# Performance work log

Measured on AMD Instinct MI355X. Metric: run time of the kernel, lower is better.

Reference implementation:

```python
import jax, jax.numpy as jnp
import numpy as np

NUM_GROUPS = 9
POWER_P = 4.0
B = 8192

def setup_inputs() -> dict:
    key = jax.random.key(0)
    k1, k2, k3 = jax.random.split(key, 3)
    return {
        "logits_tox": jax.random.normal(k1, (B, 1), dtype=jnp.float32),
        "y_tox": jax.random.uniform(k2, (B, 1), dtype=jnp.float32),
        "y_id": jax.random.uniform(k3, (B, NUM_GROUPS), dtype=jnp.float32),
    }

def reference(logits_tox, y_tox, y_id):
    logits = logits_tox[:, 0]                      # [B]
    is_toxic = y_tox[:, 0] >= 0.5                  # [B] bool
    # D[i, j] = softplus(-(logits[i] - logits[j])) = softplus(logits[j] - logits[i])
    # row index i plays the 'pos' role, column index j plays the 'neg' role.
    D = jax.nn.softplus(logits[None, :] - logits[:, None])  # [B, B]

    in_group = (y_id >= 0.5).T                     # [G, B]
    tox = is_toxic[None, :]                        # [1, B]
    dt = logits.dtype
    sub_pos = (in_group & tox).astype(dt)          # [G, B]
    sub_neg = (in_group & ~tox).astype(dt)
    bg_pos = (~in_group & tox).astype(dt)
    bg_neg = (~in_group & ~tox).astype(dt)

    # three pair types: (sub_pos, sub_neg), (bg_pos, sub_neg), (sub_pos, bg_neg)
    pos_masks = jnp.stack([sub_pos, bg_pos, sub_pos])   # [3, G, B]
    neg_masks = jnp.stack([sub_neg, sub_neg, bg_neg])   # [3, G, B]

    num = jnp.einsum('tgi,ij,tgj->tg', pos_masks, D, neg_masks)  # [3, G]
    cnt = pos_masks.sum(-1) * neg_masks.sum(-1)                  # [3, G] n_pos*n_neg
    valid = cnt > 0                                              # pair type contributes only if both sides nonempty
    type_loss = num / jnp.maximum(cnt, 1.0)

    n_valid = valid.astype(dt).sum(0)                            # [G]
    group_loss = (type_loss * valid.astype(dt)).sum(0) / jnp.maximum(n_valid, 1.0)
    gv = (n_valid > 0).astype(dt)                                # [G] group validity
    n_groups = jnp.maximum(gv.sum(), 1.0)

    # power-mean aggregation (power_p = 4 > 1)
    mean_p = (jnp.power(group_loss, POWER_P) * gv).sum() / n_groups
    loss = jnp.power(mean_p, 1.0 / POWER_P)
    return jnp.where(gv.sum() > 0, loss, jnp.array(0.0, dt))
```

## Files before the change

kernel.cpp:

```cpp
#include <hip/hip_runtime.h>
#include <math.h>

#define NG 9
#define NBLK 1024
#define JT 16
#define LOG2E 1.4426950408889634f
#define LN2   0.6931471805599453f

__global__ __launch_bounds__(256) void k_classify(
    const float* __restrict__ logits, const float* __restrict__ ytox,
    const float* __restrict__ yid, int B, int* __restrict__ cnts,
    float2* __restrict__ iLM, float2* __restrict__ jLM) {

    __shared__ int wT[4], wN[4], offT[4], offN[4], bT, bN;
    __shared__ int gT[4][NG], gN[4][NG];

    const int tid = threadIdx.x, lane = tid & 63, wave = tid >> 6;
    const int row = blockIdx.x * 256 + tid;
    const bool v = row < B;

    float l = 0.f; bool tox = false, non = false; int m = 0;
    if (v) {
        l = logits[row] * LOG2E;
        tox = ytox[row] >= 0.5f;
        non = !tox;
#pragma unroll
        for (int g = 0; g < NG; ++g)
            if (yid[row * NG + g] >= 0.5f) m |= 1 << g;
    }

    const unsigned long long bTox = __ballot(tox), bNon = __ballot(non);
    const unsigned long long lt = (1ull << lane) - 1ull;
    const int pT = __popcll(bTox & lt), pN = __popcll(bNon & lt);
    if (lane == 0) { wT[wave] = __popcll(bTox); wN[wave] = __popcll(bNon); }
#pragma unroll
    for (int g = 0; g < NG; ++g) {
        const unsigned long long bt = __ballot(tox && ((m >> g) & 1));
        const unsigned long long bn = __ballot(non && ((m >> g) & 1));
        if (lane == 0) { gT[wave][g] = __popcll(bt); gN[wave][g] = __popcll(bn); }
    }
    __syncthreads();
    if (tid == 0) {
        int a = 0, b = 0;
#pragma unroll
        for (int w = 0; w < 4; ++w) { offT[w] = a; a += wT[w]; offN[w] = b; b += wN[w]; }
        bT = atomicAdd(&cnts[0], a);
        bN = atomicAdd(&cnts[1], b);
    }
    __syncthreads();
    if (tox) iLM[bT + offT[wave] + pT] = make_float2(l, __int_as_float(m));
    if (non) jLM[bN + offN[wave] + pN] = make_float2(l, __int_as_float(m));
    if (tid < NG)
        atomicAdd(&cnts[2 + tid], gT[0][tid] + gT[1][tid] + gT[2][tid] + gT[3][tid]);
    else if (tid < 2 * NG) {
        const int g = tid - NG;
        atomicAdd(&cnts[11 + g], gN[0][g] + gN[1][g] + gN[2][g] + gN[3][g]);
    }
}

__global__ __launch_bounds__(256, 4) void k_pairs(
    const int* __restrict__ cnts, const float2* __restrict__ iLM,
    const float2* __restrict__ jLM, float* __restrict__ part) {

    __shared__ float2 jS[JT];
    __shared__ float red[4][27];
    __shared__ float acc[27];

    const int tid = threadIdx.x, lane = tid & 63, wave = tid >> 6;
    const int blk = blockIdx.x;
    const int nI = cnts[0], nJ = cnts[1];
    const int nbI = (nI + 511) >> 9;
    const int nbJ = (nJ + JT - 1) / JT;
    const int nT = nbI * nbJ;

    if (tid < 27) acc[tid] = 0.f;

    float li0 = 1e30f, li1 = 1e30f;
    int mi0 = 0, mi1 = 0;
    float Ra0 = 0.f, Ra1 = 0.f;
    float Rg0[NG], Rg1[NG];
#pragma unroll
    for (int g = 0; g < NG; ++g) { Rg0[g] = 0.f; Rg1[g] = 0.f; }

    auto flush = [&]() {
#pragma unroll
        for (int g = 0; g < NG; ++g) {
            const bool i0 = (mi0 >> g) & 1, i1 = (mi1 >> g) & 1;
            float x0 = (i0 ? Rg0[g] : 0.f) + (i1 ? Rg1[g] : 0.f);
            float x1 = (i0 ? 0.f : Rg0[g]) + (i1 ? 0.f : Rg1[g]);
            float x2 = (i0 ? (Ra0 - Rg0[g]) : 0.f) + (i1 ? (Ra1 - Rg1[g]) : 0.f);
#pragma unroll
            for (int off = 32; off > 0; off >>= 1) {
                x0 += __shfl_xor(x0, off, 64);
                x1 += __shfl_xor(x1, off, 64);
                x2 += __shfl_xor(x2, off, 64);
            }
            if (lane == 0) {
                red[wave][g] = x0; red[wave][NG + g] = x1; red[wave][2 * NG + g] = x2;
            }
        }
        __syncthreads();
        if (tid < 27)
            acc[tid] += red[0][tid] + red[1][tid] + red[2][tid] + red[3][tid];
    };

    int prev_bi = -1;
    for (int t = blk; t < nT; t += NBLK) {
        const int bi = t % nbI, bj = t / nbI;
        if (bi != prev_bi) {
            if (prev_bi >= 0) flush();
            const int k0 = (bi << 9) + tid, k1 = k0 + 256;
            const float2 a0 = (k0 < nI) ? iLM[k0] : make_float2(1e30f, 0.f);
            const float2 a1 = (k1 < nI) ? iLM[k1] : make_float2(1e30f, 0.f);
            li0 = a0.x; mi0 = __float_as_int(a0.y);
            li1 = a1.x; mi1 = __float_as_int(a1.y);
            Ra0 = 0.f; Ra1 = 0.f;
#pragma unroll
            for (int g = 0; g < NG; ++g) { Rg0[g] = 0.f; Rg1[g] = 0.f; }
            prev_bi = bi;
        }
        const int jbeg = bj * JT;
        const int jcnt = min(JT, nJ - jbeg);
        __syncthreads();
        if (tid < jcnt) jS[tid] = jLM[jbeg + tid];
        __syncthreads();
#pragma unroll 4
        for (int k = 0; k < jcnt; ++k) {
            const float2 jv = jS[k];
            const float lj = jv.x;
            const int mj = __builtin_amdgcn_readfirstlane(__float_as_int(jv.y));
            const float s0 = __builtin_amdgcn_logf(1.f + __builtin_amdgcn_exp2f(lj - li0));
            const float s1 = __builtin_amdgcn_logf(1.f + __builtin_amdgcn_exp2f(lj - li1));
            Ra0 += s0; Ra1 += s1;
#pragma unroll
            for (int g = 0; g < NG; ++g) {
                const float bg = ((mj >> g) & 1) ? 1.f : 0.f;
                Rg0[g] = fmaf(bg, s0, Rg0[g]);
                Rg1[g] = fmaf(bg, s1, Rg1[g]);
            }
        }
    }
    if (prev_bi >= 0) flush();
    if (tid < 27) part[tid * NBLK + blk] = acc[tid];
}

__global__ __launch_bounds__(512) void k_final(
    const float* __restrict__ part, const int* __restrict__ cnts,
    float* __restrict__ out) {
    __shared__ float fin[27];
    const int tid = threadIdx.x, lane = tid & 63, wave = tid >> 6;
    for (int r = wave; r < 27; r += 8) {
        float s = 0.f;
#pragma unroll
        for (int q = 0; q < NBLK / 64; ++q) s += part[r * NBLK + (q << 6) + lane];
#pragma unroll
        for (int off = 32; off > 0; off >>= 1) s += __shfl_xor(s, off, 64);
        if (lane == 0) fin[r] = s * LN2;
    }
    __syncthreads();
    if (tid == 0) {
        const long long nT = cnts[0], nN = cnts[1];
        double accd = 0.0; int ngv = 0;
        for (int g = 0; g < NG; ++g) {
            const long long cT = cnts[2 + g], cN = cnts[11 + g];
            const long long c0 = cT * cN;
            const long long c1 = (nT - cT) * cN;
            const long long c2 = cT * (nN - cN);
            const double t0 = (double)fin[g]          / (double)(c0 > 0 ? c0 : 1);
            const double t1 = (double)fin[NG + g]     / (double)(c1 > 0 ? c1 : 1);
            const double t2 = (double)fin[2 * NG + g] / (double)(c2 > 0 ? c2 : 1);
            const int nv = (c0 > 0) + (c1 > 0) + (c2 > 0);
            const double gl = ((c0 > 0 ? t0 : 0.0) + (c1 > 0 ? t1 : 0.0) +
                               (c2 > 0 ? t2 : 0.0)) / (double)(nv > 0 ? nv : 1);
            if (nv > 0) { const double g2 = gl * gl; accd += g2 * g2; ++ngv; }
        }
        const double mp = accd / (double)(ngv > 0 ? ngv : 1);
        const double loss = sqrt(sqrt(mp));
        out[0] = (float)(ngv > 0 ? loss : 0.0);
    }
}

extern "C" void kernel_launch(void* const* d_in, const int* in_sizes, int n_in,
                              void* d_out, int out_size, void* d_ws, size_t ws_size,
                              hipStream_t stream) {
    const float* logits = (const float*)d_in[0];
    const float* ytox   = (const float*)d_in[1];
    const float* yid    = (const float*)d_in[2];
    const int B = in_sizes[0];

    char* ws = (char*)d_ws;
    int*    cnts = (int*)ws;
    float2* iLM  = (float2*)(ws + 128);
    float2* jLM  = (float2*)(ws + 128 + (size_t)B * 8);
    float*  part = (float*)(ws + 128 + (size_t)B * 16);

    hipMemsetAsync(cnts, 0, 20 * sizeof(int), stream);
    k_classify<<<dim3((B + 255) / 256), dim3(256), 0, stream>>>(
        logits, ytox, yid, B, cnts, iLM, jLM);
    k_pairs<<<dim3(NBLK), dim3(256), 0, stream>>>(cnts, iLM, jLM, part);
    k_final<<<dim3(1), dim3(512), 0, stream>>>(part, cnts, (float*)d_out);
}
```

Baseline: 92.08 us.

## Fuse classify, pair and final kernels into one cooperative kernel with grid syncs

Replaces the memset and three separate launches with a single cooperative kernel. Per-chunk counts and a shared-memory prefix scan replace the global atomics, and a binary search per element maps each i/j index into chunk-local compacted storage. The j tile grows from 16 to 32. The goal is to remove launch gaps and atomic contention, at the cost of two grid-wide barriers, a serial prefix scan in every block, and binary-search overhead on each load.

```diff
diff --git a/kernel.cpp b/kernel.cpp
--- a/kernel.cpp
+++ b/kernel.cpp
@@ -1,77 +1,97 @@
 #include <hip/hip_runtime.h>
+#include <hip/hip_cooperative_groups.h>
 #include <math.h>
+
+namespace cg = cooperative_groups;
 
 #define NG 9
 #define NBLK 1024
-#define JT 16
+#define CHROWS 256
+#define NCHMAX 1024
+#define JT 32
+#define ITILE 512
 #define LOG2E 1.4426950408889634f
 #define LN2   0.6931471805599453f
 
-__global__ __launch_bounds__(256) void k_classify(
+__global__ __launch_bounds__(256, 4) void k_fused(
     const float* __restrict__ logits, const float* __restrict__ ytox,
-    const float* __restrict__ yid, int B, int* __restrict__ cnts,
-    float2* __restrict__ iLM, float2* __restrict__ jLM) {
-
-    __shared__ int wT[4], wN[4], offT[4], offN[4], bT, bN;
-    __shared__ int gT[4][NG], gN[4][NG];
-
-    const int tid = threadIdx.x, lane = tid & 63, wave = tid >> 6;
-    const int row = blockIdx.x * 256 + tid;
-    const bool v = row < B;
-
-    float l = 0.f; bool tox = false, non = false; int m = 0;
-    if (v) {
-        l = logits[row] * LOG2E;
-        tox = ytox[row] >= 0.5f;
-        non = !tox;
-#pragma unroll
-        for (int g = 0; g < NG; ++g)
-            if (yid[row * NG + g] >= 0.5f) m |= 1 << g;
-    }
-
-    const unsigned long long bTox = __ballot(tox), bNon = __ballot(non);
-    const unsigned long long lt = (1ull << lane) - 1ull;
-    const int pT = __popcll(bTox & lt), pN = __popcll(bNon & lt);
-    if (lane == 0) { wT[wave] = __popcll(bTox); wN[wave] = __popcll(bNon); }
-#pragma unroll
-    for (int g = 0; g < NG; ++g) {
-        const unsigned long long bt = __ballot(tox && ((m >> g) & 1));
-        const unsigned long long bn = __ballot(non && ((m >> g) & 1));
-        if (lane == 0) { gT[wave][g] = __popcll(bt); gN[wave][g] = __popcll(bn); }
-    }
-    __syncthreads();
-    if (tid == 0) {
-        int a = 0, b = 0;
-#pragma unroll
-        for (int w = 0; w < 4; ++w) { offT[w] = a; a += wT[w]; offN[w] = b; b += wN[w]; }
-        bT = atomicAdd(&cnts[0], a);
-        bN = atomicAdd(&cnts[1], b);
-    }
-    __syncthreads();
-    if (tox) iLM[bT + offT[wave] + pT] = make_float2(l, __int_as_float(m));
-    if (non) jLM[bN + offN[wave] + pN] = make_float2(l, __int_as_float(m));
-    if (tid < NG)
-        atomicAdd(&cnts[2 + tid], gT[0][tid] + gT[1][tid] + gT[2][tid] + gT[3][tid]);
-    else if (tid < 2 * NG) {
-        const int g = tid - NG;
-        atomicAdd(&cnts[11 + g], gN[0][g] + gN[1][g] + gN[2][g] + gN[3][g]);
-    }
-}
-
-__global__ __launch_bounds__(256, 4) void k_pairs(
-    const int* __restrict__ cnts, const float2* __restrict__ iLM,
-    const float2* __restrict__ jLM, float* __restrict__ part) {
-
+    const float* __restrict__ yid, int B,
+    int* __restrict__ cntT, int* __restrict__ cntN,
+    int* __restrict__ gTc, int* __restrict__ gNc,
+    float2* __restrict__ iTmp, float2* __restrict__ jTmp,
+    float* __restrict__ part, float* __restrict__ out) {
+
+    cg::grid_group grid = cg::this_grid();
+
+    __shared__ int offT[NCHMAX + 1], offN[NCHMAX + 1];
     __shared__ float2 jS[JT];
     __shared__ float red[4][27];
     __shared__ float acc[27];
+    __shared__ float fin[27];
+    __shared__ int cTs[NG], cNs[NG];
+    __shared__ int wcT[4], wcN[4], woT[4], woN[4];
+    __shared__ int gT[4][NG], gN[4][NG];
 
     const int tid = threadIdx.x, lane = tid & 63, wave = tid >> 6;
     const int blk = blockIdx.x;
-    const int nI = cnts[0], nJ = cnts[1];
-    const int nbI = (nI + 511) >> 9;
-    const int nbJ = (nJ + JT - 1) / JT;
-    const int nT = nbI * nbJ;
+    const int nCh = (B + CHROWS - 1) / CHROWS;
+
+    if (blk < nCh) {
+        const int row = blk * CHROWS + tid;
+        const bool v = row < B;
+        float l = 0.f; bool tox = false, non = false; int m = 0;
+        if (v) {
+            l = logits[row] * LOG2E;
+            tox = ytox[row] >= 0.5f;
+            non = !tox;
+#pragma unroll
+            for (int g = 0; g < NG; ++g)
+                if (yid[row * NG + g] >= 0.5f) m |= 1 << g;
+        }
+        const unsigned long long bTox = __ballot(tox), bNon = __ballot(non);
+        const unsigned long long lt = (1ull << lane) - 1ull;
+        const int pT = __popcll(bTox & lt), pN = __popcll(bNon & lt);
+        if (lane == 0) { wcT[wave] = __popcll(bTox); wcN[wave] = __popcll(bNon); }
+#pragma unroll
+        for (int g = 0; g < NG; ++g) {
+            const unsigned long long bt = __ballot(tox && ((m >> g) & 1));
+            const unsigned long long bn = __ballot(non && ((m >> g) & 1));
+            if (lane == 0) { gT[wave][g] = __popcll(bt); gN[wave][g] = __popcll(bn); }
+        }
+        __syncthreads();
+        if (tid == 0) {
+            int a = 0, b = 0;
+#pragma unroll
+            for (int w = 0; w < 4; ++w) { woT[w] = a; a += wcT[w]; woN[w] = b; b += wcN[w]; }
+            cntT[blk] = a; cntN[blk] = b;
+        }
+        __syncthreads();
+        if (tox) iTmp[blk * CHROWS + woT[wave] + pT] = make_float2(l, __int_as_float(m));
+        if (non) jTmp[blk * CHROWS + woN[wave] + pN] = make_float2(l, __int_as_float(m));
+        if (tid < NG)
+            gTc[blk * NG + tid] = gT[0][tid] + gT[1][tid] + gT[2][tid] + gT[3][tid];
+        else if (tid >= 64 && tid < 64 + NG) {
+            const int g = tid - 64;
+            gNc[blk * NG + g] = gN[0][g] + gN[1][g] + gN[2][g] + gN[3][g];
+        }
+        __threadfence();
+    }
+    grid.sync();
+
+    for (int c = tid; c < nCh; c += 256) { offT[c + 1] = cntT[c]; offN[c + 1] = cntN[c]; }
+    if (tid == 0) { offT[0] = 0; offN[0] = 0; }
+    __syncthreads();
+    if (tid == 0) {
+        for (int c = 0; c < nCh; ++c) { offT[c + 1] += offT[c]; offN[c + 1] += offN[c]; }
+    }
+    __syncthreads();
+    const int nI = offT[nCh], nJ = offN[nCh];
+
+    auto findChunk = [&](const int* off, int k) {
+        int lo = 0, hi = nCh;
+        while (hi - lo > 1) { const int mid = (lo + hi) >> 1; if (off[mid] <= k) lo = mid; else hi = mid; }
+        return lo;
+    };
 
     if (tid < 27) acc[tid] = 0.f;
 
@@ -104,14 +124,19 @@
             acc[tid] += red[0][tid] + red[1][tid] + red[2][tid] + red[3][tid];
     };
 
+    const int nbI = (nI + ITILE - 1) / ITILE;
+    const int nbJ = (nJ + JT - 1) / JT;
+    const int nT = nbI * nbJ;
+
     int prev_bi = -1;
     for (int t = blk; t < nT; t += NBLK) {
         const int bi = t % nbI, bj = t / nbI;
         if (bi != prev_bi) {
             if (prev_bi >= 0) flush();
-            const int k0 = (bi << 9) + tid, k1 = k0 + 256;
-            const float2 a0 = (k0 < nI) ? iLM[k0] : make_float2(1e30f, 0.f);
-            const float2 a1 = (k1 < nI) ? iLM[k1] : make_float2(1e30f, 0.f);
+            const int k0 = bi * ITILE + tid, k1 = k0 + 256;
+            float2 a0 = make_float2(1e30f, 0.f), a1 = make_float2(1e30f, 0.f);
+            if (k0 < nI) { const int c = findChunk(offT, k0); a0 = iTmp[c * CHROWS + (k0 - offT[c])]; }
+            if (k1 < nI) { const int c = findChunk(offT, k1); a1 = iTmp[c * CHROWS + (k1 - offT[c])]; }
             li0 = a0.x; mi0 = __float_as_int(a0.y);
             li1 = a1.x; mi1 = __float_as_int(a1.y);
             Ra0 = 0.f; Ra1 = 0.f;
@@ -122,7 +147,11 @@
         const int jbeg = bj * JT;
         const int jcnt = min(JT, nJ - jbeg);
         __syncthreads();
-        if (tid < jcnt) jS[tid] = jLM[jbeg + tid];
+        if (tid < jcnt) {
+            const int k = jbeg + tid;
+            const int c = findChunk(offN, k);
+            jS[tid] = jTmp[c * CHROWS + (k - offN[c])];
+        }
         __syncthreads();
 #pragma unroll 4
         for (int k = 0; k < jcnt; ++k) {
@@ -142,14 +171,12 @@
     }
     if (prev_bi >= 0) flush();
     if (tid < 27) part[tid * NBLK + blk] = acc[tid];
-}
-
-__global__ __launch_bounds__(512) void k_final(
-    const float* __restrict__ part, const int* __restrict__ cnts,
-    float* __restrict__ out) {
-    __shared__ float fin[27];
-    const int tid = threadIdx.x, lane = tid & 63, wave = tid >> 6;
-    for (int r = wave; r < 27; r += 8) {
+    __threadfence();
+    grid.sync();
+
+    if (blk != 0) return;
+
+    for (int r = wave; r < 27; r += 4) {
         float s = 0.f;
 #pragma unroll
         for (int q = 0; q < NBLK / 64; ++q) s += part[r * NBLK + (q << 6) + lane];
@@ -157,15 +184,25 @@
         for (int off = 32; off > 0; off >>= 1) s += __shfl_xor(s, off, 64);
         if (lane == 0) fin[r] = s * LN2;
     }
+    if (tid < NG) {
+        int s = 0;
+        for (int c = 0; c < nCh; ++c) s += gTc[c * NG + tid];
+        cTs[tid] = s;
+    } else if (tid >= 64 && tid < 64 + NG) {
+        const int g = tid - 64;
+        int s = 0;
+        for (int c = 0; c < nCh; ++c) s += gNc[c * NG + g];
+        cNs[g] = s;
+    }
     __syncthreads();
     if (tid == 0) {
-        const long long nT = cnts[0], nN = cnts[1];
+        const long long nT64 = nI, nN64 = nJ;
         double accd = 0.0; int ngv = 0;
         for (int g = 0; g < NG; ++g) {
-            const long long cT = cnts[2 + g], cN = cnts[11 + g];
+            const long long cT = cTs[g], cN = cNs[g];
             const long long c0 = cT * cN;
-            const long long c1 = (nT - cT) * cN;
-            const long long c2 = cT * (nN - cN);
+            const long long c1 = (nT64 - cT) * cN;
+            const long long c2 = cT * (nN64 - cN);
             const double t0 = (double)fin[g]          / (double)(c0 > 0 ? c0 : 1);
             const double t1 = (double)fin[NG + g]     / (double)(c1 > 0 ? c1 : 1);
             const double t2 = (double)fin[2 * NG + g] / (double)(c2 > 0 ? c2 : 1);
@@ -186,17 +223,21 @@
     const float* logits = (const float*)d_in[0];
     const float* ytox   = (const float*)d_in[1];
     const float* yid    = (const float*)d_in[2];
-    const int B = in_sizes[0];
+    int B = in_sizes[0];
 
     char* ws = (char*)d_ws;
-    int*    cnts = (int*)ws;
-    float2* iLM  = (float2*)(ws + 128);
-    float2* jLM  = (float2*)(ws + 128 + (size_t)B * 8);
-    float*  part = (float*)(ws + 128 + (size_t)B * 16);
-
-    hipMemsetAsync(cnts, 0, 20 * sizeof(int), stream);
-    k_classify<<<dim3((B + 255) / 256), dim3(256), 0, stream>>>(
-        logits, ytox, yid, B, cnts, iLM, jLM);
-    k_pairs<<<dim3(NBLK), dim3(256), 0, stream>>>(cnts, iLM, jLM, part);
-    k_final<<<dim3(1), dim3(512), 0, stream>>>(part, cnts, (float*)d_out);
+    int* cntT = (int*)ws;
+    int* cntN = cntT + NCHMAX;
+    int* gTc  = cntN + NCHMAX;
+    int* gNc  = gTc + NCHMAX * NG;
+    float2* iTmp = (float2*)(gNc + NCHMAX * NG);
+    float2* jTmp = iTmp + B;
+    float*  part = (float*)(jTmp + B);
+    float*  outp = (float*)d_out;
+
+    void* args[] = {(void*)&logits, (void*)&ytox, (void*)&yid, (void*)&B,
+                    (void*)&cntT, (void*)&cntN, (void*)&gTc, (void*)&gNc,
+                    (void*)&iTmp, (void*)&jTmp, (void*)&part, (void*)&outp};
+    hipLaunchCooperativeKernel((const void*)k_fused, dim3(NBLK), dim3(256),
+                               args, 0, stream);
 }
```

Result: slower. 319.6 us (+247.1%).
